# Kernel optimization log

Hardware: AMD Instinct MI355X
Metric: run time of the kernel (lower is better)

## Reference

```python
import jax, jax.numpy as jnp
import numpy as np
import math

H = 16          # num_heads
DN = 128        # qk_nope_head_dim
DR = 64         # qk_rope_head_dim
DV = 128        # v_head_dim
Q_LORA = 1536
KV_LORA = 512
EPS = 1e-6
ROPE_BASE = 10000.0
YARN_FACTOR = 16.0
ORIG_MAX = 8192


def rmsnorm(x, w):
    return x * jax.lax.rsqrt(jnp.mean(x * x, axis=-1, keepdims=True) + EPS) * w


def rotate_half(x):
    h = x.shape[-1] // 2
    return jnp.concatenate([-x[..., h:], x[..., :h]], axis=-1)


def yarn_cos_sin(L, dtype):
    # YaRN-scaled inverse frequencies (RotaryEmbedding defaults)
    pos2 = jnp.arange(0, DR, 2, dtype=jnp.float32)
    inv_freq = 1.0 / (ROPE_BASE ** (pos2 / DR))
    wavelen = 2.0 * jnp.pi / inv_freq
    # low_freq_factor=1.0, high_freq_factor=4.0
    ramp = jnp.clip((ORIG_MAX / wavelen - 1.0) / (4.0 - 1.0), 0.0, 1.0)
    inv_freq = inv_freq * (1.0 - ramp) + (inv_freq / YARN_FACTOR) * ramp
    t = jnp.arange(L, dtype=jnp.float32)
    freqs = jnp.outer(t, inv_freq)                      # [L, DR/2]
    emb = jnp.concatenate([freqs, freqs], axis=-1)      # [L, DR]
    attn_factor = 0.1 * math.log(YARN_FACTOR) + 1.0     # yarn attention scaling
    cos = (jnp.cos(emb) * attn_factor)[None, :, None, :].astype(dtype)
    sin = (jnp.sin(emb) * attn_factor)[None, :, None, :].astype(dtype)
    return cos, sin


def setup_inputs() -> dict:
    key = jax.random.key(0)
    ks = jax.random.split(key, 8)
    s = 0.02
    hid = 2048
    return {
        "x": jax.random.normal(ks[0], (2, 2048, hid), jnp.float32),
        "w_qa": jax.random.normal(ks[1], (hid, Q_LORA), jnp.float32) * s,
        "q_norm_w": jnp.ones((Q_LORA,), jnp.float32),
        "w_qb": jax.random.normal(ks[2], (Q_LORA, H * (DN + DR)), jnp.float32) * s,
        "w_kva": jax.random.normal(ks[3], (hid, KV_LORA + DR), jnp.float32) * s,
        "kv_norm_w": jnp.ones((KV_LORA,), jnp.float32),
        "w_kvb": jax.random.normal(ks[4], (KV_LORA, H * (DN + DV)), jnp.float32) * s,
        "w_o": jax.random.normal(ks[5], (H * DV, hid), jnp.float32) * s,
    }


def reference(x, w_qa, q_norm_w, w_qb, w_kva, kv_norm_w, w_kvb, w_o):
    B, L, _ = x.shape
    # --- low-rank Q path ---
    q = rmsnorm(x @ w_qa, q_norm_w) @ w_qb               # [B, L, H*(DN+DR)]
    q = q.reshape(B, L, H, DN + DR)
    q_nope, q_rope = q[..., :DN], q[..., DN:]
    # --- low-rank KV path ---
    kv = x @ w_kva                                       # [B, L, KV_LORA+DR]
    kv_c, k_rope = kv[..., :KV_LORA], kv[..., KV_LORA:]
    kv = rmsnorm(kv_c, kv_norm_w) @ w_kvb                # [B, L, H*(DN+DV)]
    kv = kv.reshape(B, L, H, DN + DV)
    k_nope, v = kv[..., :DN], kv[..., DN:]
    k_rope = jnp.broadcast_to(k_rope[:, :, None, :], (B, L, H, DR))
    # --- decoupled RoPE on rope sub-dims ---
    cos, sin = yarn_cos_sin(L, x.dtype)
    q_rope = q_rope * cos + rotate_half(q_rope) * sin
    k_rope = k_rope * cos + rotate_half(k_rope) * sin
    q = jnp.concatenate([q_nope, q_rope], axis=-1)       # [B, L, H, DN+DR]
    k = jnp.concatenate([k_nope, k_rope], axis=-1)
    # --- causal SDPA, scale = 1/sqrt(qk head dim) ---
    scale = 1.0 / math.sqrt(DN + DR)
    scores = jnp.einsum('blhd,bmhd->bhlm', q, k) * scale
    mask = jnp.tril(jnp.ones((L, L), bool))
    scores = jnp.where(mask[None, None], scores, jnp.array(-1e30, scores.dtype))
    attn = jax.nn.softmax(scores, axis=-1)
    out = jnp.einsum('bhlm,bmhd->blhd', attn, v)         # [B, L, H, DV]
    return out.reshape(B, L, H * DV) @ w_o               # [B, L, hidden]
```

## Files before the change

### kernel.cpp

```cpp
#include <hip/hip_runtime.h>
#include <hip/hip_bf16.h>
#include <math.h>

#define H_    16
#define B_    2
#define L_    2048
#define HID_  2048
#define QL_   1536
#define KVL_  512

typedef unsigned short u16;
typedef __attribute__((ext_vector_type(8))) short bf16x8;
typedef __attribute__((ext_vector_type(4))) float f32x4;

__device__ __forceinline__ float bf2f(u16 u) {
    unsigned int x = ((unsigned int)u) << 16;
    return __uint_as_float(x);
}
__device__ __forceinline__ u16 f2bf(float f) {
    __hip_bfloat16 b = __float2bfloat16(f);
    return *(u16*)&b;
}
__device__ __forceinline__ void g2l16(const void* g, void* l) {
    __builtin_amdgcn_global_load_lds(
        (const __attribute__((address_space(1))) unsigned int*)g,
        (__attribute__((address_space(3))) unsigned int*)l,
        16, 0, 0);
}
__device__ __forceinline__ int kswz(int l, int d) {
    return (((d >> 3) ^ (l & 7)) << 3) | (d & 7);
}

#define QSCALE 0.07216878364870323f

__device__ inline void yarn_cs(int l, int j, float& c, float& s)
{
    float invf = expf(-(float)(2 * j) * (9.210340371976184f / 64.f));
    float wavelen = 6.283185307179586f / invf;
    float ramp = (8192.f / wavelen - 1.f) * (1.f / 3.f);
    ramp = fminf(fmaxf(ramp, 0.f), 1.f);
    float invf2 = invf * (1.f - ramp) + invf * (1.f / 16.f) * ramp;
    float ang = (float)l * invf2;
    const float af = 1.2772588722239781f;
    c = cosf(ang) * af;
    s = sinf(ang) * af;
}

__global__ __launch_bounds__(256) void yarn_tab(float* __restrict__ tab)
{
    int idx = blockIdx.x * 256 + threadIdx.x;
    int l = idx >> 5, j = idx & 31;
    float c, s; yarn_cs(l, j, c, s);
    tab[l * 64 + j] = c;
    tab[l * 64 + 32 + j] = s;
}

__global__ __launch_bounds__(256) void cvt_bf16(
    const float* __restrict__ in, u16* __restrict__ outp)
{
    int idx = blockIdx.x * 256 + threadIdx.x;
    float4 a = ((const float4*)in)[idx * 2];
    float4 b = ((const float4*)in)[idx * 2 + 1];
    union { uint4 v; u16 s[8]; } u;
    u.s[0] = f2bf(a.x); u.s[1] = f2bf(a.y); u.s[2] = f2bf(a.z); u.s[3] = f2bf(a.w);
    u.s[4] = f2bf(b.x); u.s[5] = f2bf(b.y); u.s[6] = f2bf(b.z); u.s[7] = f2bf(b.w);
    ((uint4*)outp)[idx] = u.v;
}

__global__ __launch_bounds__(256) void wtrans(
    const float* __restrict__ W, u16* __restrict__ Wt, int K, int N,
    const float* __restrict__ wvec)
{
    __shared__ float t[64][65];
    const int n0 = blockIdx.x * 64, k0 = blockIdx.y * 64;
    const int tid = threadIdx.x;
    {
        int lr = tid >> 2, nc = (tid & 3) * 16;
        float wk = wvec ? wvec[k0 + lr] : 1.f;
        const float* src = W + (size_t)(k0 + lr) * N + n0 + nc;
#pragma unroll
        for (int j = 0; j < 16; j += 4) {
            float4 v = *(const float4*)(src + j);
            t[lr][nc + j] = v.x * wk; t[lr][nc + j + 1] = v.y * wk;
            t[lr][nc + j + 2] = v.z * wk; t[lr][nc + j + 3] = v.w * wk;
        }
    }
    __syncthreads();
    {
        int nr = tid >> 2, kc = (tid & 3) * 16;
        union { uint4 v[2]; u16 s[16]; } u;
#pragma unroll
        for (int j = 0; j < 16; ++j) u.s[j] = f2bf(t[kc + j][nr]);
        uint4* dst = (uint4*)(Wt + (size_t)(n0 + nr) * K + k0 + kc);
        dst[0] = u.v[0]; dst[1] = u.v[1];
    }
}

__global__ __launch_bounds__(256) void rowss(
    const u16* __restrict__ in, int stride, int ncols, float* __restrict__ sc)
{
    const int row = blockIdx.x, tid = threadIdx.x;
    const u16* ir = in + (size_t)row * stride;
    const int nch = ncols >> 3;
    float ss = 0.f;
    for (int c = tid; c < nch; c += 256) {
        union { uint4 v; u16 s[8]; } u;
        u.v = *(const uint4*)(ir + c * 8);
#pragma unroll
        for (int j = 0; j < 8; ++j) { float v = bf2f(u.s[j]); ss += v * v; }
    }
#pragma unroll
    for (int o = 32; o > 0; o >>= 1) ss += __shfl_xor(ss, o);
    __shared__ float red[4];
    if ((tid & 63) == 0) red[tid >> 6] = ss;
    __syncthreads();
    if (tid == 0) {
        float tot = red[0] + red[1] + red[2] + red[3];
        sc[row] = rsqrtf(tot / (float)ncols + 1e-6f);
    }
}

template<int NI> struct EpiStoreBf16 {
    u16* C; int ldc;
    __device__ void operator()(const f32x4* acc, int m0, int n0, int wr, int wc,
                               int g, int n) const {
#pragma unroll
        for (int mi = 0; mi < 4; ++mi)
#pragma unroll
            for (int ni = 0; ni < NI; ++ni)
#pragma unroll
                for (int i = 0; i < 4; ++i)
                    C[(size_t)(m0 + wr + mi * 16 + g * 4 + i) * ldc
                      + n0 + wc + ni * 16 + n] = f2bf(acc[mi * NI + ni][i]);
    }
};
template<int NI> struct EpiStoreF32 {
    float* C; int ldc;
    __device__ void operator()(const f32x4* acc, int m0, int n0, int wr, int wc,
                               int g, int n) const {
#pragma unroll
        for (int mi = 0; mi < 4; ++mi)
#pragma unroll
            for (int ni = 0; ni < NI; ++ni)
#pragma unroll
                for (int i = 0; i < 4; ++i)
                    C[(size_t)(m0 + wr + mi * 16 + g * 4 + i) * ldc
                      + n0 + wc + ni * 16 + n] = acc[mi * NI + ni][i];
    }
};
struct EpiQA {
    u16* qaR; u16* kvf;
    __device__ void operator()(const f32x4* acc, int m0, int n0, int wr, int wc,
                               int g, int n) const {
        int c0 = n0 + wc;
#pragma unroll
        for (int mi = 0; mi < 4; ++mi)
#pragma unroll
            for (int i = 0; i < 4; ++i) {
                int rr = m0 + wr + mi * 16 + g * 4 + i;
#pragma unroll
                for (int ni = 0; ni < 2; ++ni) {
                    int c = c0 + ni * 16 + n;
                    float v = acc[mi * 2 + ni][i];
                    if (c < 1536) qaR[(size_t)rr * 1536 + c] = f2bf(v);
                    else          kvf[(size_t)rr * 576 + (c - 1536)] = f2bf(v);
                }
            }
    }
};
struct EpiQ {
    u16* Qb; const float* tab; const float* sc;
    __device__ void operator()(const f32x4* acc, int m0, int n0, int wr, int wc,
                               int g, int n) const {
        int c0 = n0 + wc;
        int h = c0 / 192, r0 = c0 % 192;
#pragma unroll
        for (int mi = 0; mi < 4; ++mi)
#pragma unroll
            for (int i = 0; i < 4; ++i) {
                int rr = m0 + wr + mi * 16 + g * 4 + i;
                int b = rr >> 11, l = rr & 2047;
                float scl = sc[rr] * QSCALE;
                size_t base = ((size_t)(b * 16 + h) * 2048 + l) * 192;
                if (r0 < 128) {
#pragma unroll
                    for (int ni = 0; ni < 4; ++ni)
                        Qb[base + r0 + ni * 16 + n] = f2bf(acc[mi * 4 + ni][i] * scl);
                } else {
#pragma unroll
                    for (int ni = 0; ni < 2; ++ni) {
                        int j = ni * 16 + n;
                        float cs = tab[l * 64 + j], sn = tab[l * 64 + 32 + j];
                        float lo = acc[mi * 4 + ni][i] * scl;
                        float hi = acc[mi * 4 + ni + 2][i] * scl;
                        Qb[base + 128 + j] = f2bf(lo * cs - hi * sn);
                        Qb[base + 160 + j] = f2bf(hi * cs + lo * sn);
                    }
                }
            }
    }
};
struct EpiKV {
    u16* Kb; u16* Vc; const float* sc;
    __device__ void operator()(const f32x4* acc, int m0, int n0, int wr, int wc,
                               int g, int n) const {
        int c0 = n0 + wc;
        int h = c0 >> 8, r0 = c0 & 255;
#pragma unroll
        for (int mi = 0; mi < 4; ++mi)
#pragma unroll
            for (int i = 0; i < 4; ++i) {
                int rr = m0 + wr + mi * 16 + g * 4 + i;
                int b = rr >> 11, l = rr & 2047;
                float scl = sc[rr];
                if (r0 < 128) {
                    size_t base = ((size_t)(b * 16 + h) * 2048 + l) * 192;
#pragma unroll
                    for (int ni = 0; ni < 4; ++ni) {
                        int d = r0 + ni * 16 + n;
                        Kb[base + kswz(l, d)] = f2bf(acc[mi * 4 + ni][i] * scl);
                    }
                } else {
#pragma unroll
                    for (int ni = 0; ni < 4; ++ni)
                        Vc[(size_t)rr * 2048 + h * 128 + (r0 - 128) + ni * 16 + n]
                            = f2bf(acc[mi * 4 + ni][i] * scl);
                }
            }
    }
};

template<int BN, class Epi>
__global__ __launch_bounds__(256) void gemm_bf16(
    const u16* __restrict__ A, int lda,
    const u16* __restrict__ Bt, int ldb,
    int K, Epi epi)
{
    constexpr int NI = BN / 32;
    __shared__ u16 As[128 * 32];
    __shared__ u16 Bs[BN * 32];
    const int tid = threadIdx.x;
    const int w = tid >> 6, lane = tid & 63;
    const int g = lane >> 4, n = lane & 15;
    const int wr = (w >> 1) * 64, wc = (w & 1) * (BN / 2);
    const int nwg = gridDim.x * gridDim.y;
    const int lin = blockIdx.y * gridDim.x + blockIdx.x;
    const int swz = (lin & 7) * (nwg >> 3) + (lin >> 3);
    const int m0 = (swz / gridDim.x) * 128, n0 = (swz % gridDim.x) * BN;
    const int arow = lane >> 2, acol = (lane & 3) * 8;

    f32x4 acc[4][NI];
#pragma unroll
    for (int mi = 0; mi < 4; ++mi)
#pragma unroll
        for (int ni = 0; ni < NI; ++ni) acc[mi][ni] = (f32x4){0.f, 0.f, 0.f, 0.f};

    for (int k0 = 0; k0 < K; k0 += 32) {
        __syncthreads();
#pragma unroll
        for (int i = 0; i < 2; ++i) {
            int seg = w * 2 + i;
            int row = seg * 16 + arow;
            g2l16(A + (size_t)(m0 + row) * lda + k0 + acol, &As[seg * 512]);
        }
        if constexpr (BN == 128) {
#pragma unroll
            for (int i = 0; i < 2; ++i) {
                int seg = w * 2 + i;
                int row = seg * 16 + arow;
                g2l16(Bt + (size_t)(n0 + row) * ldb + k0 + acol, &Bs[seg * 512]);
            }
        } else {
            int row = w * 16 + arow;
            g2l16(Bt + (size_t)(n0 + row) * ldb + k0 + acol, &Bs[w * 512]);
        }
        __syncthreads();

        bf16x8 af[4], bf[NI];
#pragma unroll
        for (int mi = 0; mi < 4; ++mi)
            af[mi] = *(const bf16x8*)&As[(wr + mi * 16 + n) * 32 + g * 8];
#pragma unroll
        for (int ni = 0; ni < NI; ++ni)
            bf[ni] = *(const bf16x8*)&Bs[(wc + ni * 16 + n) * 32 + g * 8];
#pragma unroll
        for (int mi = 0; mi < 4; ++mi)
#pragma unroll
            for (int ni = 0; ni < NI; ++ni)
                acc[mi][ni] = __builtin_amdgcn_mfma_f32_16x16x32_bf16(
                    af[mi], bf[ni], acc[mi][ni], 0, 0, 0);
    }
    epi(&acc[0][0], m0, n0, wr, wc, g, n);
}

__global__ __launch_bounds__(256) void krope(
    const u16* __restrict__ kvf_b, u16* __restrict__ Kb,
    const float* __restrict__ tab)
{
    int idx = blockIdx.x * 256 + threadIdx.x;
    int j = idx & 31;
    int l = (idx >> 5) & 2047;
    int bh = idx >> 16;
    int b = bh >> 4;
    size_t row = (size_t)(b * 2048 + l);
    float x0 = bf2f(kvf_b[row * 576 + 512 + j]);
    float x1 = bf2f(kvf_b[row * 576 + 544 + j]);
    float cs = tab[l * 64 + j], sn = tab[l * 64 + 32 + j];
    size_t base = ((size_t)bh * 2048 + l) * 192;
    Kb[base + kswz(l, 128 + j)] = f2bf(x0 * cs - x1 * sn);
    Kb[base + kswz(l, 160 + j)] = f2bf(x1 * cs + x0 * sn);
}

__global__ __launch_bounds__(256) void vtrans_b(
    const u16* __restrict__ Vc, u16* __restrict__ Vt)
{
    __shared__ u16 t[64][72];
    const int tid = threadIdx.x;
    const int bh = blockIdx.z, b = bh >> 4, h = bh & 15;
    const int l0 = blockIdx.x * 64, dv0 = blockIdx.y * 64;
    {
        int lr = tid >> 2, dc = (tid & 3) * 16;
        const u16* src = Vc + (size_t)(b * 2048 + l0 + lr) * 2048 + h * 128 + dv0 + dc;
        uint4 v0 = *(const uint4*)src;
        uint4 v1 = *(const uint4*)(src + 8);
        *(uint4*)&t[lr][dc] = v0;
        *(uint4*)&t[lr][dc + 8] = v1;
    }
    __syncthreads();
    {
        int dvr = tid >> 2, lc = (tid & 3) * 16;
        union { uint4 v[2]; u16 s[16]; } u;
#pragma unroll
        for (int j = 0; j < 16; ++j) u.s[j] = t[lc + j][dvr];
        uint4* dst = (uint4*)(Vt + ((size_t)bh * 128 + dv0 + dvr) * 2048 + l0 + lc);
        dst[0] = u.v[0]; dst[1] = u.v[1];
    }
}

__global__ __launch_bounds__(256) void attn_mfma(
    const u16* __restrict__ Qb,
    const u16* __restrict__ Kb,
    const u16* __restrict__ Vt,
    u16* __restrict__ outp)
{
    __shared__ u16 Kl[64 * 192];
    __shared__ u16 Vl[128 * 64];
    __shared__ u16 Pt[4][64][20];

    const int tid = threadIdx.x;
    const int w = tid >> 6, lane = tid & 63;
    const int g = lane >> 4, n = lane & 15;
    const int n7 = n & 7;
    const int lin = blockIdx.x;
    const int xcd = lin & 7, j = lin >> 3;
    const int qt = 31 - (j >> 2);
    const int bh = xcd * 4 + (j & 3);
    const int b = bh >> 4;
    const int qb0 = qt << 6;

    const u16* KsrcBase = Kb + (size_t)bh * L_ * 192;
    const u16* VsrcBase = Vt + (size_t)bh * 128 * 2048;

    bf16x8 qf[6];
    {
        const int qrow = qb0 + w * 16 + n;
        const u16* qp = Qb + ((size_t)bh * L_ + qrow) * 192 + g * 8;
#pragma unroll
        for (int kk = 0; kk < 6; ++kk)
            qf[kk] = *(const bf16x8*)(qp + kk * 32);
    }

    f32x4 acc[8];
#pragma unroll
    for (int dt = 0; dt < 8; ++dt) acc[dt] = (f32x4){0.f, 0.f, 0.f, 0.f};
    float mi[4] = {-INFINITY, -INFINITY, -INFINITY, -INFINITY};
    float li[4] = {0.f, 0.f, 0.f, 0.f};

    const int ntiles = qt + 1;
    for (int kt = 0; kt < ntiles; ++kt) {
        const int kb = kt << 6;
        __syncthreads();
        {
            const u16* Ksrc = KsrcBase + (size_t)kb * 192;
#pragma unroll
            for (int i = 0; i < 6; ++i) {
                int c = i * 4 + w;
                g2l16(Ksrc + c * 512 + lane * 8, &Kl[c * 512]);
            }
        }
        {
#pragma unroll
            for (int i = 0; i < 4; ++i) {
                int c = i * 4 + w;
                int dv = c * 8 + (lane >> 3);
                int blk = (lane & 7) ^ (lane >> 3);
                g2l16(VsrcBase + (size_t)dv * 2048 + kb + blk * 8, &Vl[c * 512]);
            }
        }
        __syncthreads();

        f32x4 s[4];
#pragma unroll
        for (int c = 0; c < 4; ++c) s[c] = (f32x4){0.f, 0.f, 0.f, 0.f};
        __builtin_amdgcn_s_setprio(1);
#pragma unroll
        for (int c = 0; c < 4; ++c)
#pragma unroll
            for (int kk = 0; kk < 6; ++kk) {
                bf16x8 kf = *(const bf16x8*)
                    &Kl[(c * 16 + n) * 192 + ((kk * 4 + g) ^ n7) * 8];
                s[c] = __builtin_amdgcn_mfma_f32_16x16x32_bf16(qf[kk], kf, s[c], 0, 0, 0);
            }
        __builtin_amdgcn_s_setprio(0);

        const bool diag = (kt == qt);
        float al[4];
#pragma unroll
        for (int i = 0; i < 4; ++i) {
            float v[4];
            if (diag) {
                int qr = qb0 + w * 16 + g * 4 + i;
#pragma unroll
                for (int c = 0; c < 4; ++c)
                    v[c] = (kb + c * 16 + n <= qr) ? s[c][i] : -1e30f;
            } else {
#pragma unroll
                for (int c = 0; c < 4; ++c) v[c] = s[c][i];
            }
            float mx = fmaxf(fmaxf(v[0], v[1]), fmaxf(v[2], v[3]));
            mx = fmaxf(mx, __shfl_xor(mx, 1));
            mx = fmaxf(mx, __shfl_xor(mx, 2));
            mx = fmaxf(mx, __shfl_xor(mx, 4));
            mx = fmaxf(mx, __shfl_xor(mx, 8));
            float mnew = fmaxf(mi[i], mx);
            float p0 = __expf(v[0] - mnew);
            float p1 = __expf(v[1] - mnew);
            float p2 = __expf(v[2] - mnew);
            float p3 = __expf(v[3] - mnew);
            float a = __expf(mi[i] - mnew);
            li[i] = li[i] * a + ((p0 + p1) + (p2 + p3));
            mi[i] = mnew;
            al[i] = a;
            s[0][i] = p0; s[1][i] = p1; s[2][i] = p2; s[3][i] = p3;
        }
#pragma unroll
        for (int c = 0; c < 4; ++c) {
            union { double d; u16 hh[4]; } u;
#pragma unroll
            for (int i = 0; i < 4; ++i) u.hh[i] = f2bf(s[c][i]);
            *(double*)&Pt[w][c * 16 + n][g * 4] = u.d;
        }
        asm volatile("s_waitcnt lgkmcnt(0)" ::: "memory");
        __builtin_amdgcn_sched_barrier(0);

        union { bf16x8 v; short e[8]; } pf[2];
#pragma unroll
        for (int ks = 0; ks < 2; ++ks)
#pragma unroll
            for (int jj = 0; jj < 8; ++jj)
                pf[ks].e[jj] = *(const short*)&Pt[w][ks * 32 + g * 8 + jj][n];

        __builtin_amdgcn_s_setprio(1);
#pragma unroll
        for (int dt = 0; dt < 8; ++dt) {
#pragma unroll
            for (int i = 0; i < 4; ++i) acc[dt][i] *= al[i];
#pragma unroll
            for (int ks = 0; ks < 2; ++ks) {
                bf16x8 vf = *(const bf16x8*)
                    &Vl[(dt * 16 + n) * 64 + (((ks * 4 + g) ^ n7) << 3)];
                acc[dt] = __builtin_amdgcn_mfma_f32_16x16x32_bf16(pf[ks].v, vf, acc[dt], 0, 0, 0);
            }
        }
        __builtin_amdgcn_s_setprio(0);
    }

    float inv[4];
#pragma unroll
    for (int i = 0; i < 4; ++i) {
        float t = li[i];
        t += __shfl_xor(t, 1);
        t += __shfl_xor(t, 2);
        t += __shfl_xor(t, 4);
        t += __shfl_xor(t, 8);
        inv[i] = __frcp_rn(t);
    }
#pragma unroll
    for (int dt = 0; dt < 8; ++dt) {
#pragma unroll
        for (int i = 0; i < 4; ++i) {
            int qr = qb0 + w * 16 + g * 4 + i;
            outp[(size_t)(b * L_ + qr) * 2048 + (bh & 15) * 128 + dt * 16 + n]
                = f2bf(acc[dt][i] * inv[i]);
        }
    }
}

extern "C" void kernel_launch(void* const* d_in, const int* in_sizes, int n_in,
                              void* d_out, int out_size, void* d_ws, size_t ws_size,
                              hipStream_t stream)
{
    const float* x     = (const float*)d_in[0];
    const float* w_qa  = (const float*)d_in[1];
    const float* qnw   = (const float*)d_in[2];
    const float* w_qb  = (const float*)d_in[3];
    const float* w_kva = (const float*)d_in[4];
    const float* kvnw  = (const float*)d_in[5];
    const float* w_kvb = (const float*)d_in[6];
    const float* w_o   = (const float*)d_in[7];
    float* out = (float*)d_out;
    u16* W = (u16*)d_ws;

    const size_t o_wt_qa  = 0;
    const size_t o_wt_kva = o_wt_qa  + (size_t)1536 * 2048;
    const size_t o_wt_qb  = o_wt_kva + (size_t)576 * 2048;
    const size_t o_wt_kvb = o_wt_qb  + (size_t)3072 * 1536;
    const size_t o_wt_o   = o_wt_kvb + (size_t)4096 * 512;
    const size_t o_tab    = o_wt_o   + (size_t)2048 * 2048;
    const size_t o_sc     = o_tab    + 262144;
    const size_t o_Qb     = o_sc     + 16384;
    const size_t o_Kb     = o_Qb     + 12582912;
    const size_t o_Vt     = o_Kb     + 12582912;
    const size_t o_Vc     = o_Vt     + 8388608;
    const size_t o_xb     = o_Vc     + 8388608;

    u16* Wt_qa  = W + o_wt_qa;
    u16* Wt_kva = W + o_wt_kva;
    u16* Wt_qb  = W + o_wt_qb;
    u16* Wt_kvb = W + o_wt_kvb;
    u16* Wt_o   = W + o_wt_o;
    float* tab  = (float*)(W + o_tab);
    float* sc_q  = (float*)(W + o_sc);
    float* sc_kv = sc_q + 4096;
    u16* Qb     = W + o_Qb;
    u16* qaR_b  = W + o_Kb;
    u16* Kb     = W + o_Kb;
    u16* kvf_b  = W + o_Vt;
    u16* Vt     = W + o_Vt;
    u16* Vc     = W + o_Vc;
    u16* atto_b = W + o_Vc;
    u16* x_b    = W + o_xb;

    dim3 blk(256);

    yarn_tab<<<(2048 * 32) / 256, blk, 0, stream>>>(tab);
    cvt_bf16<<<4096, blk, 0, stream>>>(x, x_b);
    wtrans<<<dim3(1536 / 64, 2048 / 64), blk, 0, stream>>>(w_qa,  Wt_qa,  2048, 1536, nullptr);
    wtrans<<<dim3( 576 / 64, 2048 / 64), blk, 0, stream>>>(w_kva, Wt_kva, 2048, 576,  nullptr);
    wtrans<<<dim3(3072 / 64, 1536 / 64), blk, 0, stream>>>(w_qb,  Wt_qb,  1536, 3072, qnw);
    wtrans<<<dim3(4096 / 64,  512 / 64), blk, 0, stream>>>(w_kvb, Wt_kvb, 512, 4096,  kvnw);
    wtrans<<<dim3(2048 / 64, 2048 / 64), blk, 0, stream>>>(w_o,   Wt_o,   2048, 2048, nullptr);

    gemm_bf16<64, EpiQA><<<dim3(33, 32), blk, 0, stream>>>(
        x_b, 2048, Wt_qa, 2048, 2048, EpiQA{qaR_b, kvf_b});
    rowss<<<4096, blk, 0, stream>>>(qaR_b, 1536, 1536, sc_q);
    rowss<<<4096, blk, 0, stream>>>(kvf_b, 576, 512, sc_kv);
    gemm_bf16<128, EpiQ><<<dim3(24, 32), blk, 0, stream>>>(
        qaR_b, 1536, Wt_qb, 1536, 1536, EpiQ{Qb, tab, sc_q});
    gemm_bf16<128, EpiKV><<<dim3(32, 32), blk, 0, stream>>>(
        kvf_b, 576, Wt_kvb, 512, 512, EpiKV{Kb, Vc, sc_kv});
    krope<<<(32 * 2048 * 32) / 256, blk, 0, stream>>>(kvf_b, Kb, tab);
    vtrans_b<<<dim3(32, 2, 32), blk, 0, stream>>>(Vc, Vt);

    attn_mfma<<<dim3(1024), blk, 0, stream>>>(Qb, Kb, Vt, atto_b);
    gemm_bf16<64, EpiStoreF32<2>><<<dim3(32, 32), blk, 0, stream>>>(
        atto_b, 2048, Wt_o, 2048, 2048, EpiStoreF32<2>{out, 2048});
}
```

Baseline: 367.4 us.

## Pair causal query tiles per 512-thread block and use lazy softmax rescaling

The attention kernel now runs 8 waves per block, pairing a long query tile (31-pr) with a short one (pr) so each block shares the K/V tile loads and the causal work is balanced. Waves whose rows are fully masked skip compute after the shared load. Softmax moves to exp2 with log2e folded into the Q scale, and it only rescales the accumulator when the running max grows by more than a threshold. This cuts the exp and multiply work per tile. The cost is larger blocks with higher register pressure, and wasted load bandwidth for the short-tile waves.

```diff
diff --git a/kernel.cpp b/kernel.cpp
--- a/kernel.cpp
+++ b/kernel.cpp
@@ -31,7 +31,13 @@
     return (((d >> 3) ^ (l & 7)) << 3) | (d & 7);
 }
 
-#define QSCALE 0.07216878364870323f
+#if __has_builtin(__builtin_amdgcn_exp2f)
+#define EXP2F __builtin_amdgcn_exp2f
+#else
+#define EXP2F exp2f
+#endif
+
+#define QSCALE (0.07216878364870323f * 1.4426950408889634f)
 
 __device__ inline void yarn_cs(int l, int j, float& c, float& s)
 {
@@ -120,20 +126,6 @@
     }
 }
 
-template<int NI> struct EpiStoreBf16 {
-    u16* C; int ldc;
-    __device__ void operator()(const f32x4* acc, int m0, int n0, int wr, int wc,
-                               int g, int n) const {
-#pragma unroll
-        for (int mi = 0; mi < 4; ++mi)
-#pragma unroll
-            for (int ni = 0; ni < NI; ++ni)
-#pragma unroll
-                for (int i = 0; i < 4; ++i)
-                    C[(size_t)(m0 + wr + mi * 16 + g * 4 + i) * ldc
-                      + n0 + wc + ni * 16 + n] = f2bf(acc[mi * NI + ni][i]);
-    }
-};
 template<int NI> struct EpiStoreF32 {
     float* C; int ldc;
     __device__ void operator()(const f32x4* acc, int m0, int n0, int wr, int wc,
@@ -337,7 +329,7 @@
     }
 }
 
-__global__ __launch_bounds__(256) void attn_mfma(
+__global__ __launch_bounds__(512, 4) void attn_mfma(
     const u16* __restrict__ Qb,
     const u16* __restrict__ Kb,
     const u16* __restrict__ Vt,
@@ -345,25 +337,27 @@
 {
     __shared__ u16 Kl[64 * 192];
     __shared__ u16 Vl[128 * 64];
-    __shared__ u16 Pt[4][64][20];
+    __shared__ u16 Pt[8][64][20];
 
     const int tid = threadIdx.x;
     const int w = tid >> 6, lane = tid & 63;
     const int g = lane >> 4, n = lane & 15;
     const int n7 = n & 7;
     const int lin = blockIdx.x;
-    const int xcd = lin & 7, j = lin >> 3;
-    const int qt = 31 - (j >> 2);
-    const int bh = xcd * 4 + (j & 3);
+    const int xcd = lin & 7;
+    const int bh  = xcd * 4 + ((lin >> 3) & 3);
+    const int pr  = lin >> 5;
+    const int qt  = (w < 4) ? (31 - pr) : pr;
+    const int wq  = w & 3;
+    const int qb0 = qt << 6;
     const int b = bh >> 4;
-    const int qb0 = qt << 6;
 
     const u16* KsrcBase = Kb + (size_t)bh * L_ * 192;
     const u16* VsrcBase = Vt + (size_t)bh * 128 * 2048;
 
     bf16x8 qf[6];
     {
-        const int qrow = qb0 + w * 16 + n;
+        const int qrow = qb0 + wq * 16 + n;
         const u16* qp = Qb + ((size_t)bh * L_ + qrow) * 192 + g * 8;
 #pragma unroll
         for (int kk = 0; kk < 6; ++kk)
@@ -376,28 +370,32 @@
     float mi[4] = {-INFINITY, -INFINITY, -INFINITY, -INFINITY};
     float li[4] = {0.f, 0.f, 0.f, 0.f};
 
-    const int ntiles = qt + 1;
+    const int myqmax = qb0 + wq * 16 + 15;
+    const int ntiles = 32 - pr;
+
     for (int kt = 0; kt < ntiles; ++kt) {
         const int kb = kt << 6;
         __syncthreads();
         {
             const u16* Ksrc = KsrcBase + (size_t)kb * 192;
 #pragma unroll
-            for (int i = 0; i < 6; ++i) {
-                int c = i * 4 + w;
+            for (int i = 0; i < 3; ++i) {
+                int c = i * 8 + w;
                 g2l16(Ksrc + c * 512 + lane * 8, &Kl[c * 512]);
             }
         }
         {
 #pragma unroll
-            for (int i = 0; i < 4; ++i) {
-                int c = i * 4 + w;
+            for (int i = 0; i < 2; ++i) {
+                int c = i * 8 + w;
                 int dv = c * 8 + (lane >> 3);
                 int blk = (lane & 7) ^ (lane >> 3);
                 g2l16(VsrcBase + (size_t)dv * 2048 + kb + blk * 8, &Vl[c * 512]);
             }
         }
         __syncthreads();
+
+        if (kb > myqmax) continue;
 
         f32x4 s[4];
 #pragma unroll
@@ -413,35 +411,55 @@
             }
         __builtin_amdgcn_s_setprio(0);
 
-        const bool diag = (kt == qt);
-        float al[4];
+        if (kb + 63 > qb0 + wq * 16) {
+#pragma unroll
+            for (int i = 0; i < 4; ++i) {
+                int qr = qb0 + wq * 16 + g * 4 + i;
+#pragma unroll
+                for (int c = 0; c < 4; ++c)
+                    if (kb + c * 16 + n > qr) s[c][i] = -1e30f;
+            }
+        }
+        float mx[4];
+        bool need = false;
 #pragma unroll
         for (int i = 0; i < 4; ++i) {
-            float v[4];
-            if (diag) {
-                int qr = qb0 + w * 16 + g * 4 + i;
-#pragma unroll
-                for (int c = 0; c < 4; ++c)
-                    v[c] = (kb + c * 16 + n <= qr) ? s[c][i] : -1e30f;
-            } else {
-#pragma unroll
-                for (int c = 0; c < 4; ++c) v[c] = s[c][i];
-            }
-            float mx = fmaxf(fmaxf(v[0], v[1]), fmaxf(v[2], v[3]));
-            mx = fmaxf(mx, __shfl_xor(mx, 1));
-            mx = fmaxf(mx, __shfl_xor(mx, 2));
-            mx = fmaxf(mx, __shfl_xor(mx, 4));
-            mx = fmaxf(mx, __shfl_xor(mx, 8));
-            float mnew = fmaxf(mi[i], mx);
-            float p0 = __expf(v[0] - mnew);
-            float p1 = __expf(v[1] - mnew);
-            float p2 = __expf(v[2] - mnew);
-            float p3 = __expf(v[3] - mnew);
-            float a = __expf(mi[i] - mnew);
-            li[i] = li[i] * a + ((p0 + p1) + (p2 + p3));
-            mi[i] = mnew;
-            al[i] = a;
-            s[0][i] = p0; s[1][i] = p1; s[2][i] = p2; s[3][i] = p3;
+            float m = fmaxf(fmaxf(s[0][i], s[1][i]), fmaxf(s[2][i], s[3][i]));
+            m = fmaxf(m, __shfl_xor(m, 1));
+            m = fmaxf(m, __shfl_xor(m, 2));
+            m = fmaxf(m, __shfl_xor(m, 4));
+            m = fmaxf(m, __shfl_xor(m, 8));
+            mx[i] = m;
+            need |= (m > mi[i] + 8.f);
+        }
+        if (__ballot(need) != 0ULL) {
+            float al[4];
+#pragma unroll
+            for (int i = 0; i < 4; ++i) {
+                float mnew = fmaxf(mi[i], mx[i]);
+                float a = EXP2F(mi[i] - mnew);
+                float p0 = EXP2F(s[0][i] - mnew);
+                float p1 = EXP2F(s[1][i] - mnew);
+                float p2 = EXP2F(s[2][i] - mnew);
+                float p3 = EXP2F(s[3][i] - mnew);
+                li[i] = li[i] * a + ((p0 + p1) + (p2 + p3));
+                mi[i] = mnew; al[i] = a;
+                s[0][i] = p0; s[1][i] = p1; s[2][i] = p2; s[3][i] = p3;
+            }
+#pragma unroll
+            for (int dt = 0; dt < 8; ++dt)
+#pragma unroll
+                for (int i = 0; i < 4; ++i) acc[dt][i] *= al[i];
+        } else {
+#pragma unroll
+            for (int i = 0; i < 4; ++i) {
+                float p0 = EXP2F(s[0][i] - mi[i]);
+                float p1 = EXP2F(s[1][i] - mi[i]);
+                float p2 = EXP2F(s[2][i] - mi[i]);
+                float p3 = EXP2F(s[3][i] - mi[i]);
+                li[i] += (p0 + p1) + (p2 + p3);
+                s[0][i] = p0; s[1][i] = p1; s[2][i] = p2; s[3][i] = p3;
+            }
         }
 #pragma unroll
         for (int c = 0; c < 4; ++c) {
@@ -462,16 +480,13 @@
 
         __builtin_amdgcn_s_setprio(1);
 #pragma unroll
-        for (int dt = 0; dt < 8; ++dt) {
-#pragma unroll
-            for (int i = 0; i < 4; ++i) acc[dt][i] *= al[i];
+        for (int dt = 0; dt < 8; ++dt)
 #pragma unroll
             for (int ks = 0; ks < 2; ++ks) {
                 bf16x8 vf = *(const bf16x8*)
                     &Vl[(dt * 16 + n) * 64 + (((ks * 4 + g) ^ n7) << 3)];
                 acc[dt] = __builtin_amdgcn_mfma_f32_16x16x32_bf16(pf[ks].v, vf, acc[dt], 0, 0, 0);
             }
-        }
         __builtin_amdgcn_s_setprio(0);
     }
 
@@ -489,7 +504,7 @@
     for (int dt = 0; dt < 8; ++dt) {
 #pragma unroll
         for (int i = 0; i < 4; ++i) {
-            int qr = qb0 + w * 16 + g * 4 + i;
+            int qr = qb0 + wq * 16 + g * 4 + i;
             outp[(size_t)(b * L_ + qr) * 2048 + (bh & 15) * 128 + dt * 16 + n]
                 = f2bf(acc[dt][i] * inv[i]);
         }
@@ -562,7 +577,7 @@
     krope<<<(32 * 2048 * 32) / 256, blk, 0, stream>>>(kvf_b, Kb, tab);
     vtrans_b<<<dim3(32, 2, 32), blk, 0, stream>>>(Vc, Vt);
 
-    attn_mfma<<<dim3(1024), blk, 0, stream>>>(Qb, Kb, Vt, atto_b);
+    attn_mfma<<<dim3(512), dim3(512), 0, stream>>>(Qb, Kb, Vt, atto_b);
     gemm_bf16<64, EpiStoreF32<2>><<<dim3(32, 32), blk, 0, stream>>>(
         atto_b, 2048, Wt_o, 2048, 2048, EpiStoreF32<2>{out, 2048});
 }
```

Result: slower. 447.9 us (+21.9%).
